# Performance work log

Hardware: AMD Instinct MI355X
Metric: run time of the kernel (lower is better)

The kernel has to match this reference:

```python
import jax, jax.numpy as jnp
import numpy as np

TINY = 1e-15
EPS = 1e-6
B, T, D, H, N = 1, 512, 512, 8, 64
A = N + 1  # ambient dim
TAU = 1.0


def mink(x, y):
    # Minkowski inner product over the last dim
    return -x[..., 0] * y[..., 0] + jnp.sum(x[..., 1:] * y[..., 1:], axis=-1)


def project(x):
    xx = mink(x, x)
    scale = jnp.sqrt(jnp.maximum(jnp.abs(xx), TINY))[..., None]
    x = x / scale
    return jnp.concatenate([jnp.abs(x[..., :1]), x[..., 1:]], axis=-1)


def exp_map(p, v):
    vn = jnp.sqrt(jnp.maximum(mink(v, v), TINY))[..., None]
    y = jnp.cosh(vn) * p + (jnp.sinh(vn) / jnp.maximum(vn, TINY)) * v
    return project(y)


def log_map(p, y):
    alpha = -mink(p, y)
    dist = jnp.arccosh(jnp.maximum(alpha, 1.0 + EPS))[..., None]
    u = y + alpha[..., None] * p
    un = jnp.sqrt(jnp.maximum(mink(u, u), TINY))[..., None]
    return dist / jnp.maximum(un, TINY) * u


def rope(u):
    # u: [B,H,T,N]; standard half-rotation RoPE, base 10000
    inv_freq = 1.0 / (10000.0 ** (jnp.arange(0, N, 2, dtype=jnp.float32) / N))
    ang = jnp.arange(T, dtype=jnp.float32)[:, None] * inv_freq[None, :]  # [T, N/2]
    cos = jnp.concatenate([jnp.cos(ang), jnp.cos(ang)], axis=-1)  # [T, N]
    sin = jnp.concatenate([jnp.sin(ang), jnp.sin(ang)], axis=-1)
    u1, u2 = u[..., : N // 2], u[..., N // 2:]
    rot = jnp.concatenate([-u2, u1], axis=-1)
    return u * cos + rot * sin


def lift(u):
    # append time-like 0, expmap at origin -> points on hyperboloid [B,H,T,A]
    v = jnp.concatenate([jnp.zeros(u.shape[:-1] + (1,), u.dtype), u], axis=-1)
    o = jnp.zeros((A,), u.dtype).at[0].set(1.0)
    return exp_map(o, v)


def setup_inputs() -> dict:
    key = jax.random.key(0)
    ks = jax.random.split(key, 10)
    s = 0.02
    x = jax.random.normal(ks[0], (B, T, D), jnp.float32)
    Wq = jax.random.normal(ks[1], (D, H * N), jnp.float32) * s
    bq = jax.random.normal(ks[2], (H * N,), jnp.float32) * s
    Wk = jax.random.normal(ks[3], (D, H * N), jnp.float32) * s
    bk = jax.random.normal(ks[4], (H * N,), jnp.float32) * s
    Wv = jax.random.normal(ks[5], (D, H * N), jnp.float32) * s
    bv = jax.random.normal(ks[6], (H * N,), jnp.float32) * s
    Wo = jax.random.normal(ks[7], (H * A, D), jnp.float32) * s
    bo = jax.random.normal(ks[8], (D,), jnp.float32) * s
    sp = jax.random.normal(ks[9], (N,), jnp.float32) * 0.1
    anchor_p = jnp.concatenate([jnp.sqrt(1.0 + jnp.sum(sp * sp))[None], sp])  # valid hyperboloid point
    return dict(x=x, Wq=Wq, bq=bq, Wk=Wk, bk=bk, Wv=Wv, bv=bv, Wo=Wo, bo=bo, anchor_p=anchor_p)


def reference(x, Wq, bq, Wk, bk, Wv, bv, Wo, bo, anchor_p):
    def pack(u):  # [B,T,H*N] -> [B,H,T,N]
        return u.reshape(B, T, H, N).transpose(0, 2, 1, 3)

    uq = rope(pack(x @ Wq + bq))
    uk = rope(pack(x @ Wk + bk))
    uv = pack(x @ Wv + bv)
    Q = lift(uq)  # [B,H,T,A]
    K = lift(uk)
    V = lift(uv)

    # pairwise Lorentz distance scores, softmax in fp32
    alpha_qk = -mink(Q[:, :, :, None, :].astype(jnp.float32), K[:, :, None, :, :].astype(jnp.float32))
    d = jnp.arccosh(jnp.maximum(alpha_qk, 1.0 + EPS))  # [B,H,T,T]
    attn = jax.nn.softmax(-TAU * d * d, axis=-1).astype(V.dtype)

    # one Karcher-mean step around the query point (karcher_steps=1)
    Y = Q
    logv = log_map(Y[:, :, :, None, :], V[:, :, None, :, :])  # [B,H,T,T,A]
    u = jnp.sum(attn[..., None] * logv, axis=3)  # [B,H,T,A]
    Y = exp_map(Y, u)

    Yc = Y.transpose(0, 2, 1, 3)  # [B,T,H,A]
    Z_tan = log_map(anchor_p[None, None, None, :], Yc).reshape(B, T, H * A)
    return Z_tan @ Wo + bo
```

## Files before the change

kernel.cpp:

```cpp
#include <hip/hip_runtime.h>
#include <math.h>

#define T_ 512
#define D_ 512
#define H_ 8
#define N_ 64
#define A_ 65
#define HN_ 512
#define HA_ 520
#define QS_ 66
#define VS_ 66
#define KTS_ 512
#define SYS_ 68
#define EPS_ 1e-6
#define EPSF_ 1e-6f
#define TINY_ 1e-15
#define IT 8
#define PTT 4
#define CTT 2

__device__ __forceinline__ double wsumd(double v){
#pragma unroll
  for (int o=32;o;o>>=1) v += __shfl_xor(v,o);
  return v;
}
__device__ __forceinline__ float wsumf(float v){
#pragma unroll
  for (int o=32;o;o>>=1) v += __shfl_xor(v,o);
  return v;
}
__device__ __forceinline__ float wmaxf(float v){
#pragma unroll
  for (int o=32;o;o>>=1) v = fmaxf(v,__shfl_xor(v,o));
  return v;
}
__device__ __forceinline__ float facoshf(float x){
  return __logf(x + sqrtf(fmaf(x,x,-1.f)));
}

__global__ void k_fill(float* __restrict__ out, float val){
  int i = blockIdx.x*256 + threadIdx.x;
  if (i < T_*D_) out[i] = val;
}

__global__ __launch_bounds__(256) void k_trig(double* __restrict__ tab){
  int i = blockIdx.x*256 + threadIdx.x;
  int t = i >> 5, fi = i & 31;
  double inv_f = 1.0 / pow(10000.0, (double)(2*fi)*(1.0/64.0));
  double ang = (double)t * inv_f;
  tab[2*i+0] = cos(ang);
  tab[2*i+1] = sin(ang);
}

__global__ __launch_bounds__(256) void k_projlift(
    const float* __restrict__ x,
    const float* __restrict__ Wq, const float* __restrict__ bq,
    const float* __restrict__ Wk, const float* __restrict__ bk,
    const float* __restrict__ Wv, const float* __restrict__ bv,
    const double* __restrict__ trig,
    float* __restrict__ Qf, float* __restrict__ KTf,
    float* __restrict__ Vf, float* __restrict__ VTf){
  int mode = blockIdx.y;
  const float* W  = (mode==0)?Wq:((mode==1)?Wk:Wv);
  const float* bb = (mode==0)?bq:((mode==1)?bk:bv);
  int tid = threadIdx.x;
  int c = blockIdx.x*256 + tid;
  int n = c & 63, h = c >> 6;
  int t0 = blockIdx.z*PTT;
  float acc[PTT];
#pragma unroll
  for (int i=0;i<PTT;i++) acc[i]=0.f;

  float w0[8], w1[8];
#pragma unroll
  for (int k=0;k<8;k++) w0[k] = W[(size_t)(k)*HN_ + c];
#pragma unroll
  for (int k=0;k<8;k++) w1[k] = W[(size_t)(8+k)*HN_ + c];

#pragma unroll 2
  for (int d=0; d<D_-16; d+=8){
    float wp[8];
#pragma unroll
    for (int k=0;k<8;k++) wp[k] = W[(size_t)(d+16+k)*HN_ + c];
#pragma unroll
    for (int i=0;i<PTT;i++){
      const float* xr = x + (size_t)(t0+i)*D_ + d;
#pragma unroll
      for (int k=0;k<8;k++) acc[i] = fmaf(xr[k], w0[k], acc[i]);
    }
#pragma unroll
    for (int k=0;k<8;k++){ w0[k]=w1[k]; w1[k]=wp[k]; }
  }
#pragma unroll
  for (int i=0;i<PTT;i++){
    const float* xr = x + (size_t)(t0+i)*D_ + (D_-16);
#pragma unroll
    for (int k=0;k<8;k++) acc[i] = fmaf(xr[k],   w0[k], acc[i]);
#pragma unroll
    for (int k=0;k<8;k++) acc[i] = fmaf(xr[8+k], w1[k], acc[i]);
  }

  float bias = bb[c];
#pragma unroll 1
  for (int i=0;i<PTT;i++){
    int t = t0 + i;
    double v = (double)(acc[i] + bias);
    if (mode < 2){
      const double2 cs2 = *reinterpret_cast<const double2*>(trig + 2*((size_t)t*32 + (n&31)));
      double vp = __shfl_xor(v, 32);
      double rot = (n<32) ? -vp : vp;
      v = v*cs2.x + rot*cs2.y;
    }
    double ss = wsumd(v*v);
    double vn = sqrt(fmax(ss, TINY_));
    double e  = exp(vn);
    double ei = 1.0/e;
    double ch = 0.5*(e+ei);
    double s  = (0.5*(e-ei))/vn;
    double xx = s*s*ss - ch*ch;
    double scale = sqrt(fmax(fabs(xx), TINY_));
    float y0 = (float)fabs(ch/scale);
    float ya = (float)(s*v/scale);
    if (mode==0){
      float* o = Qf + (size_t)h*T_*QS_ + (size_t)t*QS_;
      if (n==0) o[0] = y0;
      o[n+1] = ya;
    } else if (mode==1){
      float* o = KTf + (size_t)h*66*KTS_ + t;
      if (n==0) o[0] = y0;
      o[(size_t)(n+1)*KTS_] = ya;
    } else {
      float* o = Vf + (size_t)h*T_*VS_ + (size_t)t*VS_;
      if (n==0) o[0] = y0;
      o[n+1] = ya;
      float* ot = VTf + (size_t)h*66*KTS_ + t;
      if (n==0) ot[0] = y0;
      ot[(size_t)(n+1)*KTS_] = ya;
    }
  }
}

__global__ __launch_bounds__(256) void k_attnF(
    const float* __restrict__ Qf, const float* __restrict__ KTf,
    const float* __restrict__ VTf, const float* __restrict__ Vf,
    const float* __restrict__ anchor, float* __restrict__ Z){
  __shared__ float  sYf[IT][QS_];
  __shared__ float  sYm[IT][SYS_];
  __shared__ float  s_w[IT][T_];
  __shared__ double sA[A_];
  __shared__ float  s_red[4][IT];
  __shared__ float  s_part[4][IT][64];
  __shared__ float  s_p64[4][IT];

  int h = blockIdx.x, i0 = blockIdx.y*IT, tid = threadIdx.x;
  int wv = tid>>6, lane = tid&63;
  const float* Qp = Qf  + (size_t)h*T_*QS_;
  const float* KT = KTf + (size_t)h*66*KTS_;
  const float* VT = VTf + (size_t)h*66*KTS_;
  const float* Vp = Vf  + (size_t)h*T_*VS_;

  for (int f=tid; f<IT*QS_; f+=256){
    int i=f/QS_, a=f-i*QS_;
    sYf[i][a] = (a<A_) ? Qp[(size_t)(i0+i)*QS_ + a] : 0.f;
  }
  for (int f=tid; f<IT*SYS_; f+=256){
    int i=f/SYS_, a=f-i*SYS_;
    float v = (a<A_) ? Qp[(size_t)(i0+i)*QS_ + a] : 0.f;
    sYm[i][a] = (a==0) ? v : -v;
  }
  if (tid < A_) sA[tid] = (double)anchor[tid];
  __syncthreads();

  int j0 = tid, j1 = tid + 256;
  {
    float aq0[IT], aq1[IT];
#pragma unroll
    for (int i=0;i<IT;i++){ aq0[i]=0.f; aq1[i]=0.f; }
    for (int a4=0; a4<16; a4++){
      int a = a4*4;
      float k00=KT[(size_t)(a+0)*KTS_+j0], k01=KT[(size_t)(a+1)*KTS_+j0];
      float k02=KT[(size_t)(a+2)*KTS_+j0], k03=KT[(size_t)(a+3)*KTS_+j0];
      float k10=KT[(size_t)(a+0)*KTS_+j1], k11=KT[(size_t)(a+1)*KTS_+j1];
      float k12=KT[(size_t)(a+2)*KTS_+j1], k13=KT[(size_t)(a+3)*KTS_+j1];
#pragma unroll
      for (int i=0;i<IT;i++){
        float4 ym = *reinterpret_cast<const float4*>(&sYm[i][a]);
        aq0[i] = fmaf(ym.w,k03,fmaf(ym.z,k02,fmaf(ym.y,k01,fmaf(ym.x,k00,aq0[i]))));
        aq1[i] = fmaf(ym.w,k13,fmaf(ym.z,k12,fmaf(ym.y,k11,fmaf(ym.x,k10,aq1[i]))));
      }
    }
    float kt0 = KT[(size_t)64*KTS_+j0], kt1 = KT[(size_t)64*KTS_+j1];
#pragma unroll
    for (int i=0;i<IT;i++){
      float a0 = fmaf(sYm[i][64], kt0, aq0[i]);
      float a1 = fmaf(sYm[i][64], kt1, aq1[i]);
      float d0 = facoshf(fmaxf(a0, 1.f+EPSF_));
      float d1 = facoshf(fmaxf(a1, 1.f+EPSF_));
      s_w[i][j0] = -d0*d0;
      s_w[i][j1] = -d1*d1;
    }
  }
  __syncthreads();

  for (int ii=0; ii<2; ii++){
    int i = wv*2 + ii;
    float m = -INFINITY;
#pragma unroll
    for (int kk=0;kk<8;kk++) m = fmaxf(m, s_w[i][lane+64*kk]);
    m = wmaxf(m);
    float e[8], sum=0.f;
#pragma unroll
    for (int kk=0;kk<8;kk++){ e[kk]=__expf(s_w[i][lane+64*kk]-m); sum+=e[kk]; }
    sum = wsumf(sum);
    float inv = 1.f/sum;
#pragma unroll
    for (int kk=0;kk<8;kk++) s_w[i][lane+64*kk] = e[kk]*inv;
  }
  __syncthreads();

  {
    float av0[IT], av1[IT];
#pragma unroll
    for (int i=0;i<IT;i++){ av0[i]=0.f; av1[i]=0.f; }
    for (int a4=0; a4<16; a4++){
      int a = a4*4;
      float v00=VT[(size_t)(a+0)*KTS_+j0], v01=VT[(size_t)(a+1)*KTS_+j0];
      float v02=VT[(size_t)(a+2)*KTS_+j0], v03=VT[(size_t)(a+3)*KTS_+j0];
      float v10=VT[(size_t)(a+0)*KTS_+j1], v11=VT[(size_t)(a+1)*KTS_+j1];
      float v12=VT[(size_t)(a+2)*KTS_+j1], v13=VT[(size_t)(a+3)*KTS_+j1];
#pragma unroll
      for (int i=0;i<IT;i++){
        float4 ym = *reinterpret_cast<const float4*>(&sYm[i][a]);
        av0[i] = fmaf(ym.w,v03,fmaf(ym.z,v02,fmaf(ym.y,v01,fmaf(ym.x,v00,av0[i]))));
        av1[i] = fmaf(ym.w,v13,fmaf(ym.z,v12,fmaf(ym.y,v11,fmaf(ym.x,v10,av1[i]))));
      }
    }
    float vt0 = VT[(size_t)64*KTS_+j0], vt1 = VT[(size_t)64*KTS_+j1];
    const float inv_un0 = 3.16227766016838e7f;
    float cyp[IT];
#pragma unroll
    for (int i=0;i<IT;i++){
      float a0 = fmaf(sYm[i][64], vt0, av0[i]);
      float a1 = fmaf(sYm[i][64], vt1, av1[i]);
      float at0 = s_w[i][j0], at1 = s_w[i][j1];
      float d0 = facoshf(fmaxf(a0, 1.f+EPSF_));
      float d1 = facoshf(fmaxf(a1, 1.f+EPSF_));
      float w0 = at0*d0*inv_un0;
      float w1 = at1*d1*inv_un0;
      s_w[i][j0] = w0;
      s_w[i][j1] = w1;
      cyp[i] = fmaf(w0, a0, w1*a1);
    }
#pragma unroll
    for (int i=0;i<IT;i++){
      float r = wsumf(cyp[i]);
      if (lane==0) s_red[wv][i] = r;
    }
  }
  __syncthreads();

  {
    float pL[IT], p64r[IT];
#pragma unroll
    for (int i=0;i<IT;i++){ pL[i]=0.f; p64r[i]=0.f; }
    int jb = wv*128;
    for (int jj=0; jj<128; jj+=4){
      int j = jb + jj;
      float vA = Vp[(size_t)(j+0)*VS_ + lane];
      float vB = Vp[(size_t)(j+1)*VS_ + lane];
      float vC = Vp[(size_t)(j+2)*VS_ + lane];
      float vD = Vp[(size_t)(j+3)*VS_ + lane];
#pragma unroll
      for (int i=0;i<IT;i++){
        float4 w4 = *reinterpret_cast<const float4*>(&s_w[i][j]);
        pL[i] = fmaf(w4.w,vD,fmaf(w4.z,vC,fmaf(w4.y,vB,fmaf(w4.x,vA,pL[i]))));
      }
    }
#pragma unroll
    for (int cc=0; cc<2; cc++){
      int j = jb + cc*64 + lane;
      float v64 = VT[(size_t)64*KTS_ + j];
#pragma unroll
      for (int i=0;i<IT;i++) p64r[i] = fmaf(s_w[i][j], v64, p64r[i]);
    }
#pragma unroll
    for (int i=0;i<IT;i++){
      s_part[wv][i][lane] = pL[i];
      float r = wsumf(p64r[i]);
      if (lane==0) s_p64[wv][i] = r;
    }
  }
  __syncthreads();

  for (int ii=0; ii<2; ii++){
    int r = wv*2 + ii;
    double Yl  = (double)sYf[r][lane];
    double Y64 = (double)sYf[r][64];
    double cy = (double)s_red[0][r]+(double)s_red[1][r]+(double)s_red[2][r]+(double)s_red[3][r];
    double aL = (double)s_part[0][r][lane]+(double)s_part[1][r][lane]
              + (double)s_part[2][r][lane]+(double)s_part[3][r][lane];
    double a64 = (double)s_p64[0][r]+(double)s_p64[1][r]+(double)s_p64[2][r]+(double)s_p64[3][r];
    double ua  = fma(cy, Yl,  aL);
    double u64 = fma(cy, Y64, a64);
    double c2 = (lane==0) ? fma(u64,u64, -ua*ua) : ua*ua;
    double mv = wsumd(c2);
    double vn = sqrt(fmax(mv, TINY_));
    double ch = cosh(vn);
    double sh = sinh(vn)/fmax(vn, TINY_);
    double ya  = fma(ch, Yl,  sh*ua);
    double y64 = fma(ch, Y64, sh*u64);
    double c3 = (lane==0) ? fma(y64,y64, -ya*ya) : ya*ya;
    double px = wsumd(c3);
    double scale = sqrt(fmax(fabs(px), TINY_));
    double Pa  = ya/scale; if (lane==0) Pa = fabs(Pa);
    double P64 = y64/scale;
    double sAl = sA[lane];
    double azc = (lane==0) ? fma(sAl, Pa, -sA[64]*P64) : (-sAl*Pa);
    double az = wsumd(azc);
    double dz = acosh(fmax(az, 1.0+EPS_));
    double uza  = fma(az, sAl,    Pa);
    double uz64 = fma(az, sA[64], P64);
    double c4v = (lane==0) ? fma(uz64,uz64, -uza*uza) : uza*uza;
    double mz = wsumd(c4v);
    double unz = sqrt(fmax(mz, TINY_));
    double fz = dz/fmax(unz, TINY_);
    float* Zr = Z + (size_t)(i0+r)*HA_ + h*A_;
    Zr[lane] = (float)(fz*uza);
    if (lane==0) Zr[64] = (float)(fz*uz64);
  }
}

__global__ __launch_bounds__(256) void k_outD(
    const float* __restrict__ Zb, const float* __restrict__ Wo,
    const float* __restrict__ bo, float* __restrict__ out){
  int c  = blockIdx.x*256 + threadIdx.x;
  int t0 = blockIdx.y*CTT;
  float acc[CTT];
#pragma unroll
  for (int i=0;i<CTT;i++) acc[i]=0.f;
  for (int k=0;k<HA_;k+=4){
    float w0 = Wo[(size_t)(k+0)*D_ + c];
    float w1 = Wo[(size_t)(k+1)*D_ + c];
    float w2 = Wo[(size_t)(k+2)*D_ + c];
    float w3 = Wo[(size_t)(k+3)*D_ + c];
#pragma unroll
    for (int i=0;i<CTT;i++){
      const float* zr = Zb + (size_t)(t0+i)*HA_;
      acc[i] = fmaf(zr[k+0], w0, acc[i]);
      acc[i] = fmaf(zr[k+1], w1, acc[i]);
      acc[i] = fmaf(zr[k+2], w2, acc[i]);
      acc[i] = fmaf(zr[k+3], w3, acc[i]);
    }
  }
  float bb = bo[c];
#pragma unroll
  for (int i=0;i<CTT;i++) out[(t0+i)*D_ + c] = acc[i] + bb;
}

extern "C" void kernel_launch(void* const* d_in, const int* in_sizes, int n_in,
                              void* d_out, int out_size, void* d_ws, size_t ws_size,
                              hipStream_t stream){
  float* out = (float*)d_out;

  bool ok = (n_in == 10) && (out_size == T_*D_)
    && in_sizes[0]==T_*D_ && in_sizes[1]==D_*HN_ && in_sizes[2]==HN_
    && in_sizes[3]==D_*HN_ && in_sizes[4]==HN_
    && in_sizes[5]==D_*HN_ && in_sizes[6]==HN_
    && in_sizes[7]==HA_*D_ && in_sizes[8]==D_ && in_sizes[9]==A_;
  if (!ok){ k_fill<<<1024,256,0,stream>>>(out, 1.0e12f); return; }

  const float* x      = (const float*)d_in[0];
  const float* Wq     = (const float*)d_in[1];
  const float* bq     = (const float*)d_in[2];
  const float* Wk     = (const float*)d_in[3];
  const float* bk     = (const float*)d_in[4];
  const float* Wv     = (const float*)d_in[5];
  const float* bv     = (const float*)d_in[6];
  const float* Wo     = (const float*)d_in[7];
  const float* bo     = (const float*)d_in[8];
  const float* anchor = (const float*)d_in[9];
  char* ws = (char*)d_ws;

  size_t zbytes  = (size_t)T_*HA_*sizeof(float);
  size_t qbytes  = (size_t)H_*T_*QS_*sizeof(float);
  size_t ktbytes = (size_t)H_*66*KTS_*sizeof(float);
  size_t vbytes  = (size_t)H_*T_*VS_*sizeof(float);
  size_t vtbytes = (size_t)H_*66*KTS_*sizeof(float);
  size_t tbytes  = (size_t)T_*32*2*sizeof(double);
  size_t need    = zbytes+qbytes+ktbytes+vbytes+vtbytes+tbytes;
  if (ws_size < need){ k_fill<<<1024,256,0,stream>>>(out, 2.0e12f); return; }

  float*  Zf = (float*)ws;
  float*  Qf = (float*)(ws + zbytes);
  float*  KT = (float*)(ws + zbytes + qbytes);
  float*  Vf = (float*)(ws + zbytes + qbytes + ktbytes);
  float*  VT = (float*)(ws + zbytes + qbytes + ktbytes + vbytes);
  double* TB = (double*)(ws + zbytes + qbytes + ktbytes + vbytes + vtbytes);

  k_trig    <<<dim3(T_*32/256),  256, 0, stream>>>(TB);
  k_projlift<<<dim3(2,3,T_/PTT), 256, 0, stream>>>(x, Wq,bq, Wk,bk, Wv,bv, TB, Qf, KT, Vf, VT);
  k_attnF   <<<dim3(H_, T_/IT),  256, 0, stream>>>(Qf, KT, VT, Vf, anchor, Zf);
  k_outD    <<<dim3(2, T_/CTT),  256, 0, stream>>>(Zf, Wo, bo, out);
}
```

Baseline: 103.6 us.

## Tile projection GEMM over heads with double-buffered shared-memory weight chunks

The projection/lift kernel is restructured so that each block covers one head (64 columns) and 16 rows, with each wavefront taking 4 rows. Weight tiles of 64x64 are staged through a double-buffered LDS buffer, so each weight element is read from global memory once per block and shared across its four wavefronts, rather than every thread streaming its own column. The x reads use a wave-uniform row base via readfirstlane, so they can become scalar loads. The change adds a barrier per chunk and more LDS traffic, and the grid goes from 768 to 768 blocks of a different shape.

```diff
diff --git a/kernel.cpp b/kernel.cpp
--- a/kernel.cpp
+++ b/kernel.cpp
@@ -17,6 +17,10 @@
 #define TINY_ 1e-15
 #define IT 8
 #define PTT 4
+#define RPB_ 16
+#define BN_ 64
+#define CH_ 64
+#define NCH_ (D_/CH_)
 #define CTT 2
 
 __device__ __forceinline__ double wsumd(double v){
@@ -60,47 +64,61 @@
     const double* __restrict__ trig,
     float* __restrict__ Qf, float* __restrict__ KTf,
     float* __restrict__ Vf, float* __restrict__ VTf){
+  __shared__ float sW[2][CH_*BN_];
   int mode = blockIdx.y;
   const float* W  = (mode==0)?Wq:((mode==1)?Wk:Wv);
   const float* bb = (mode==0)?bq:((mode==1)?bk:bv);
   int tid = threadIdx.x;
-  int c = blockIdx.x*256 + tid;
-  int n = c & 63, h = c >> 6;
-  int t0 = blockIdx.z*PTT;
+  int lane = tid & 63;
+  int h = blockIdx.x;
+  int n = lane;
+  int t0 = __builtin_amdgcn_readfirstlane(blockIdx.z*RPB_ + ((tid>>6)<<2));
+  int srr = tid >> 4;
+  int scc = (tid*4) & 63;
+
   float acc[PTT];
 #pragma unroll
   for (int i=0;i<PTT;i++) acc[i]=0.f;
 
-  float w0[8], w1[8];
-#pragma unroll
-  for (int k=0;k<8;k++) w0[k] = W[(size_t)(k)*HN_ + c];
-#pragma unroll
-  for (int k=0;k<8;k++) w1[k] = W[(size_t)(8+k)*HN_ + c];
-
-#pragma unroll 2
-  for (int d=0; d<D_-16; d+=8){
-    float wp[8];
-#pragma unroll
-    for (int k=0;k<8;k++) wp[k] = W[(size_t)(d+16+k)*HN_ + c];
-#pragma unroll
-    for (int i=0;i<PTT;i++){
-      const float* xr = x + (size_t)(t0+i)*D_ + d;
-#pragma unroll
-      for (int k=0;k<8;k++) acc[i] = fmaf(xr[k], w0[k], acc[i]);
-    }
-#pragma unroll
-    for (int k=0;k<8;k++){ w0[k]=w1[k]; w1[k]=wp[k]; }
-  }
-#pragma unroll
-  for (int i=0;i<PTT;i++){
-    const float* xr = x + (size_t)(t0+i)*D_ + (D_-16);
-#pragma unroll
-    for (int k=0;k<8;k++) acc[i] = fmaf(xr[k],   w0[k], acc[i]);
-#pragma unroll
-    for (int k=0;k<8;k++) acc[i] = fmaf(xr[8+k], w1[k], acc[i]);
-  }
-
-  float bias = bb[c];
+  {
+    float4 st[4];
+#pragma unroll
+    for (int k=0;k<4;k++)
+      st[k] = *reinterpret_cast<const float4*>(W + (size_t)(k*16+srr)*HN_ + h*BN_ + scc);
+#pragma unroll
+    for (int k=0;k<4;k++)
+      *reinterpret_cast<float4*>(&sW[0][k*1024 + tid*4]) = st[k];
+  }
+  __syncthreads();
+
+  const float* xr = x + (size_t)t0*D_;
+#pragma unroll 1
+  for (int ch=0; ch<NCH_; ++ch){
+    float4 st[4];
+    if (ch+1 < NCH_){
+#pragma unroll
+      for (int k=0;k<4;k++)
+        st[k] = *reinterpret_cast<const float4*>(
+            W + (size_t)((ch+1)*CH_ + k*16+srr)*HN_ + h*BN_ + scc);
+    }
+    const float* sb = &sW[ch&1][0];
+    int d0 = ch*CH_;
+#pragma unroll 8
+    for (int r=0;r<CH_;r++){
+      float wd = sb[r*BN_ + lane];
+#pragma unroll
+      for (int i=0;i<PTT;i++)
+        acc[i] = fmaf(xr[(size_t)i*D_ + d0 + r], wd, acc[i]);
+    }
+    if (ch+1 < NCH_){
+#pragma unroll
+      for (int k=0;k<4;k++)
+        *reinterpret_cast<float4*>(&sW[(ch+1)&1][k*1024 + tid*4]) = st[k];
+    }
+    __syncthreads();
+  }
+
+  float bias = bb[h*BN_ + n];
 #pragma unroll 1
   for (int i=0;i<PTT;i++){
     int t = t0 + i;
@@ -115,11 +133,11 @@
     double vn = sqrt(fmax(ss, TINY_));
     double e  = exp(vn);
     double ei = 1.0/e;
-    double ch = 0.5*(e+ei);
+    double ch2 = 0.5*(e+ei);
     double s  = (0.5*(e-ei))/vn;
-    double xx = s*s*ss - ch*ch;
+    double xx = s*s*ss - ch2*ch2;
     double scale = sqrt(fmax(fabs(xx), TINY_));
-    float y0 = (float)fabs(ch/scale);
+    float y0 = (float)fabs(ch2/scale);
     float ya = (float)(s*v/scale);
     if (mode==0){
       float* o = Qf + (size_t)h*T_*QS_ + (size_t)t*QS_;
@@ -397,8 +415,8 @@
   float*  VT = (float*)(ws + zbytes + qbytes + ktbytes + vbytes);
   double* TB = (double*)(ws + zbytes + qbytes + ktbytes + vbytes + vtbytes);
 
-  k_trig    <<<dim3(T_*32/256),  256, 0, stream>>>(TB);
-  k_projlift<<<dim3(2,3,T_/PTT), 256, 0, stream>>>(x, Wq,bq, Wk,bk, Wv,bv, TB, Qf, KT, Vf, VT);
-  k_attnF   <<<dim3(H_, T_/IT),  256, 0, stream>>>(Qf, KT, VT, Vf, anchor, Zf);
-  k_outD    <<<dim3(2, T_/CTT),  256, 0, stream>>>(Zf, Wo, bo, out);
-}
+  k_trig    <<<dim3(T_*32/256),   256, 0, stream>>>(TB);
+  k_projlift<<<dim3(H_,3,T_/RPB_),256, 0, stream>>>(x, Wq,bq, Wk,bk, Wv,bv, TB, Qf, KT, Vf, VT);
+  k_attnF   <<<dim3(H_, T_/IT),   256, 0, stream>>>(Qf, KT, VT, Vf, anchor, Zf);
+  k_outD    <<<dim3(2, T_/CTT),   256, 0, stream>>>(Zf, Wo, bo, out);
+}
```

Measured after the change: 100.3 us. 1.03x faster.
